# Performance work log

Hardware: AMD Instinct MI355X
Metric: run time of the kernel (lower is better)

The kernel has to match this reference:

```python
import jax, jax.numpy as jnp
import numpy as np

# CSV_Architecture_v2 layout (per frame, 130 floats):
#   hand 0 block: [0]=handedness label, [1]=handedness prob, [2:65]=21*3 coords
#   hand 1 block: [65]=handedness label, [66]=handedness prob, [67:130]=coords
POS0, PROB0 = 0, 1
POS1, PROB1 = 65, 66
HAND_LEN = 65
FRAME_LEN = 2 * HAND_LEN


def _build_swap_pattern():
    all_idxs = np.arange(FRAME_LEN)
    idxs_0 = np.arange(0, HAND_LEN)
    idxs_1 = np.arange(HAND_LEN, FRAME_LEN)
    all_idxs[idxs_0], all_idxs[idxs_1] = all_idxs[idxs_1].copy(), all_idxs[idxs_0].copy()
    return jnp.asarray(all_idxs, dtype=jnp.int32)


def setup_inputs() -> dict:
    key = jax.random.key(0)
    B, S = 256, 1024
    X = jax.random.normal(key, (B, S, FRAME_LEN), dtype=jnp.float32)
    return {"X": X, "swap_pattern": _build_swap_pattern()}


def reference(X, swap_pattern):
    # Per-frame handedness labels / probabilities.
    h0 = X[..., POS0]
    h1 = X[..., POS1]
    p0 = X[..., PROB0]
    p1 = X[..., PROB1]

    nan0 = jnp.isnan(h0)
    nan1 = jnp.isnan(h1)
    no_nan = jnp.logical_and(~nan0, ~nan1)

    one = jnp.float32(1.0)
    zero = jnp.float32(0.0)

    # skip1: hands already ordered (right label > left label)
    skip1 = h1 > h0
    # skip2: both predictions NaN -> no hands detected
    skip2 = jnp.logical_and(nan0, nan1)
    # skip3: only hand 1 present, labeled right (==1)
    skip3 = jnp.logical_and(nan0, h1 == one)
    # skip4: only hand 0 present, labeled left (==0)
    skip4 = jnp.logical_and(nan1, h0 == zero)
    eq = h0 == h1
    # skip5: both labeled left, position-0 hand has higher prob
    skip5 = no_nan & eq & (h0 == zero) & (p0 > p1)
    # skip6: both labeled right, position-1 hand has higher prob
    skip6 = no_nan & eq & (h0 == one) & (p0 < p1)

    skip = skip1 | skip2 | skip3 | skip4 | skip5 | skip6

    # Vectorized replacement of nested tf.map_fn: gather-permute the frame
    # representation where a swap is required.
    swapped = X[..., swap_pattern]  # [B, S, FRAME_LEN]
    return jnp.where(skip[..., None], X, swapped)
```

## Files before the change

kernel.cpp:

```cpp
#include <hip/hip_runtime.h>

constexpr int FRAME_LEN = 130;
constexpr int HALF      = 65;
constexpr int BLOCK     = 256;
constexpr int FPB       = 32;
constexpr int CHUNK_F   = FPB * FRAME_LEN;
constexpr int CHUNK_V4  = CHUNK_F / 4;

__device__ __forceinline__ int div130(int idx) {
    return (int)(((unsigned)idx * 8067u) >> 20);
}

__global__ __launch_bounds__(BLOCK, 8)
void hand_sorter_kernel(const float* __restrict__ X, float* __restrict__ out,
                        int n_frames) {
    __shared__ float s_buf[CHUNK_F];
    __shared__ unsigned char s_skip[FPB];

    const int t = threadIdx.x;
    const long long frame0 = (long long)blockIdx.x * FPB;
    const long long rem = (long long)n_frames - frame0;
    const int frames_here = rem < (long long)FPB ? (int)rem : FPB;
    const int nf = frames_here * FRAME_LEN;
    const int n4 = (nf + 3) >> 2;
    const long long base = frame0 * (long long)FRAME_LEN;
    const float4* __restrict__ Xv = (const float4*)(X + base);
    float4* __restrict__ Ov = (float4*)(out + base);

    for (int i = t; i < n4; i += BLOCK) {
        *(float4*)(s_buf + 4 * i) = Xv[i];
    }
    __syncthreads();

    if (t < frames_here) {
        const float* fr = s_buf + t * FRAME_LEN;
        const float h0 = fr[0];
        const float p0 = fr[1];
        const float h1 = fr[HALF];
        const float p1 = fr[HALF + 1];
        const bool nan0 = (h0 != h0);
        const bool nan1 = (h1 != h1);
        const bool no_nan = !nan0 && !nan1;
        const bool eq = (h0 == h1);
        const bool skip =
            (h1 > h0) ||
            (nan0 && nan1) ||
            (nan0 && (h1 == 1.0f)) ||
            (nan1 && (h0 == 0.0f)) ||
            (no_nan && eq && (h0 == 0.0f) && (p0 > p1)) ||
            (no_nan && eq && (h0 == 1.0f) && (p0 < p1));
        s_skip[t] = (unsigned char)skip;
    }
    __syncthreads();

    for (int i = t; i < n4; i += BLOCK) {
        const int idx = 4 * i;
        float4 v;
        float* vp = (float*)&v;
        if (idx + 3 < nf) {
#pragma unroll
            for (int e = 0; e < 4; ++e) {
                const int ide = idx + e;
                const int fl = div130(ide);
                const int jj = ide - fl * FRAME_LEN;
                int sj = jj + (s_skip[fl] ? 0 : HALF);
                if (sj >= FRAME_LEN) sj -= FRAME_LEN;
                vp[e] = s_buf[fl * FRAME_LEN + sj];
            }
            Ov[i] = v;
        } else {
            for (int e = 0; e < 4; ++e) {
                const int ide = idx + e;
                if (ide < nf) {
                    const int fl = div130(ide);
                    const int jj = ide - fl * FRAME_LEN;
                    int sj = jj + (s_skip[fl] ? 0 : HALF);
                    if (sj >= FRAME_LEN) sj -= FRAME_LEN;
                    out[base + ide] = s_buf[fl * FRAME_LEN + sj];
                }
            }
        }
    }
}

extern "C" void kernel_launch(void* const* d_in, const int* in_sizes, int n_in,
                              void* d_out, int out_size, void* d_ws, size_t ws_size,
                              hipStream_t stream) {
    const float* X = (const float*)d_in[0];
    float* out = (float*)d_out;
    const int n_frames = in_sizes[0] / FRAME_LEN;
    const int n_blocks = (n_frames + FPB - 1) / FPB;
    hand_sorter_kernel<<<n_blocks, BLOCK, 0, stream>>>(X, out, n_frames);
}
```

Measured before the change: 240.1 us.

## Drop shared-memory staging and gather directly from global memory

```diff
diff --git a/kernel.cpp b/kernel.cpp
--- a/kernel.cpp
+++ b/kernel.cpp
@@ -5,7 +5,8 @@
 constexpr int BLOCK     = 256;
 constexpr int FPB       = 32;
 constexpr int CHUNK_F   = FPB * FRAME_LEN;
-constexpr int CHUNK_V4  = CHUNK_F / 4;
+
+typedef float f4u __attribute__((ext_vector_type(4), aligned(4)));
 
 __device__ __forceinline__ int div130(int idx) {
     return (int)(((unsigned)idx * 8067u) >> 20);
@@ -14,8 +15,7 @@
 __global__ __launch_bounds__(BLOCK, 8)
 void hand_sorter_kernel(const float* __restrict__ X, float* __restrict__ out,
                         int n_frames) {
-    __shared__ float s_buf[CHUNK_F];
-    __shared__ unsigned char s_skip[FPB];
+    __shared__ int s_off[FPB];
 
     const int t = threadIdx.x;
     const long long frame0 = (long long)blockIdx.x * FPB;
@@ -24,16 +24,11 @@
     const int nf = frames_here * FRAME_LEN;
     const int n4 = (nf + 3) >> 2;
     const long long base = frame0 * (long long)FRAME_LEN;
-    const float4* __restrict__ Xv = (const float4*)(X + base);
-    float4* __restrict__ Ov = (float4*)(out + base);
-
-    for (int i = t; i < n4; i += BLOCK) {
-        *(float4*)(s_buf + 4 * i) = Xv[i];
-    }
-    __syncthreads();
+    const float* __restrict__ Xb = X + base;
+    float* __restrict__ Ob = out + base;
 
     if (t < frames_here) {
-        const float* fr = s_buf + t * FRAME_LEN;
+        const float* fr = Xb + t * FRAME_LEN;
         const float h0 = fr[0];
         const float p0 = fr[1];
         const float h1 = fr[HALF];
@@ -49,34 +44,34 @@
             (nan1 && (h0 == 0.0f)) ||
             (no_nan && eq && (h0 == 0.0f) && (p0 > p1)) ||
             (no_nan && eq && (h0 == 1.0f) && (p0 < p1));
-        s_skip[t] = (unsigned char)skip;
+        s_off[t] = skip ? 0 : HALF;
     }
     __syncthreads();
 
     for (int i = t; i < n4; i += BLOCK) {
         const int idx = 4 * i;
-        float4 v;
-        float* vp = (float*)&v;
-        if (idx + 3 < nf) {
+        const int fl = div130(idx);
+        const int jj = idx - fl * FRAME_LEN;
+        const bool same_frame = (idx + 3 < nf) && (jj <= FRAME_LEN - 4);
+        const bool no_half_cross = (jj < HALF - 3) || (jj >= HALF);
+        if (same_frame && no_half_cross) {
+            int sj = jj + s_off[fl];
+            if (sj >= FRAME_LEN) sj -= FRAME_LEN;
+            const float* src = Xb + (fl * FRAME_LEN + sj);
+            f4u v = *(const f4u*)src;
+            float4 o;
+            o.x = v.x; o.y = v.y; o.z = v.z; o.w = v.w;
+            *(float4*)(Ob + idx) = o;
+        } else {
 #pragma unroll
             for (int e = 0; e < 4; ++e) {
                 const int ide = idx + e;
-                const int fl = div130(ide);
-                const int jj = ide - fl * FRAME_LEN;
-                int sj = jj + (s_skip[fl] ? 0 : HALF);
-                if (sj >= FRAME_LEN) sj -= FRAME_LEN;
-                vp[e] = s_buf[fl * FRAME_LEN + sj];
-            }
-            Ov[i] = v;
-        } else {
-            for (int e = 0; e < 4; ++e) {
-                const int ide = idx + e;
                 if (ide < nf) {
-                    const int fl = div130(ide);
-                    const int jj = ide - fl * FRAME_LEN;
-                    int sj = jj + (s_skip[fl] ? 0 : HALF);
+                    const int fle = div130(ide);
+                    const int je = ide - fle * FRAME_LEN;
+                    int sj = je + s_off[fle];
                     if (sj >= FRAME_LEN) sj -= FRAME_LEN;
-                    out[base + ide] = s_buf[fl * FRAME_LEN + sj];
+                    Ob[ide] = Xb[fle * FRAME_LEN + sj];
                 }
             }
         }
```

Measured after the change: 268.9 us. 1.12x slower.

## Load tiles with direct global-to-LDS DMA and compute skip mask via per-wave ballot

Applied to the files above, without the earlier changes.

```diff
diff --git a/kernel.cpp b/kernel.cpp
--- a/kernel.cpp
+++ b/kernel.cpp
@@ -1,4 +1,5 @@
 #include <hip/hip_runtime.h>
+#include <stdint.h>
 
 constexpr int FRAME_LEN = 130;
 constexpr int HALF      = 65;
@@ -7,78 +8,107 @@
 constexpr int CHUNK_F   = FPB * FRAME_LEN;
 constexpr int CHUNK_V4  = CHUNK_F / 4;
 
+#define GLOBAL_AS __attribute__((address_space(1)))
+#define LDS_AS    __attribute__((address_space(3)))
+
 __device__ __forceinline__ int div130(int idx) {
     return (int)(((unsigned)idx * 8067u) >> 20);
+}
+
+__device__ __forceinline__ bool skip_pred(float h0, float p0, float h1, float p1) {
+    const bool nan0 = (h0 != h0);
+    const bool nan1 = (h1 != h1);
+    const bool no_nan = !nan0 && !nan1;
+    const bool eq = (h0 == h1);
+    return (h1 > h0) ||
+           (nan0 && nan1) ||
+           (nan0 && (h1 == 1.0f)) ||
+           (nan1 && (h0 == 0.0f)) ||
+           (no_nan && eq && (h0 == 0.0f) && (p0 > p1)) ||
+           (no_nan && eq && (h0 == 1.0f) && (p0 < p1));
 }
 
 __global__ __launch_bounds__(BLOCK, 8)
 void hand_sorter_kernel(const float* __restrict__ X, float* __restrict__ out,
                         int n_frames) {
     __shared__ float s_buf[CHUNK_F];
-    __shared__ unsigned char s_skip[FPB];
 
     const int t = threadIdx.x;
     const long long frame0 = (long long)blockIdx.x * FPB;
     const long long rem = (long long)n_frames - frame0;
     const int frames_here = rem < (long long)FPB ? (int)rem : FPB;
-    const int nf = frames_here * FRAME_LEN;
-    const int n4 = (nf + 3) >> 2;
     const long long base = frame0 * (long long)FRAME_LEN;
-    const float4* __restrict__ Xv = (const float4*)(X + base);
-    float4* __restrict__ Ov = (float4*)(out + base);
+    const float* __restrict__ Xb = X + base;
+    float* __restrict__ Ob = out + base;
 
-    for (int i = t; i < n4; i += BLOCK) {
-        *(float4*)(s_buf + 4 * i) = Xv[i];
-    }
-    __syncthreads();
+    if (frames_here == FPB) {
+        const int wbase = t & ~63;
+#pragma unroll
+        for (int k = 0; k < 4; ++k) {
+            const float* src = Xb + 4 * (k * 256 + t);
+            float* dst = s_buf + 4 * (k * 256 + wbase);
+            __builtin_amdgcn_global_load_lds(
+                (const GLOBAL_AS uint32_t*)src, (LDS_AS uint32_t*)dst, 16, 0, 0);
+        }
+        if (t < CHUNK_V4 - 1024) {
+            const float* src = Xb + 4 * (1024 + t);
+            float* dst = s_buf + 4 * 1024;
+            __builtin_amdgcn_global_load_lds(
+                (const GLOBAL_AS uint32_t*)src, (LDS_AS uint32_t*)dst, 16, 0, 0);
+        }
+        __syncthreads();
 
-    if (t < frames_here) {
-        const float* fr = s_buf + t * FRAME_LEN;
-        const float h0 = fr[0];
-        const float p0 = fr[1];
-        const float h1 = fr[HALF];
-        const float p1 = fr[HALF + 1];
-        const bool nan0 = (h0 != h0);
-        const bool nan1 = (h1 != h1);
-        const bool no_nan = !nan0 && !nan1;
-        const bool eq = (h0 == h1);
-        const bool skip =
-            (h1 > h0) ||
-            (nan0 && nan1) ||
-            (nan0 && (h1 == 1.0f)) ||
-            (nan1 && (h0 == 0.0f)) ||
-            (no_nan && eq && (h0 == 0.0f) && (p0 > p1)) ||
-            (no_nan && eq && (h0 == 1.0f) && (p0 < p1));
-        s_skip[t] = (unsigned char)skip;
-    }
-    __syncthreads();
+        const int lane = t & 63;
+        bool pred = false;
+        if (lane < FPB) {
+            const float* fr = s_buf + lane * FRAME_LEN;
+            pred = skip_pred(fr[0], fr[1], fr[HALF], fr[HALF + 1]);
+        }
+        const unsigned mask = (unsigned)__ballot(pred);
 
-    for (int i = t; i < n4; i += BLOCK) {
-        const int idx = 4 * i;
-        float4 v;
-        float* vp = (float*)&v;
-        if (idx + 3 < nf) {
+        float4* __restrict__ Ov = (float4*)Ob;
+#pragma unroll
+        for (int k = 0; k < 4; ++k) {
+            const int i = t + k * 256;
+            const int idx = 4 * i;
+            float4 v;
+            float* vp = (float*)&v;
 #pragma unroll
             for (int e = 0; e < 4; ++e) {
                 const int ide = idx + e;
                 const int fl = div130(ide);
                 const int jj = ide - fl * FRAME_LEN;
-                int sj = jj + (s_skip[fl] ? 0 : HALF);
+                int sj = jj + (((mask >> fl) & 1u) ? 0 : HALF);
                 if (sj >= FRAME_LEN) sj -= FRAME_LEN;
                 vp[e] = s_buf[fl * FRAME_LEN + sj];
             }
             Ov[i] = v;
-        } else {
+        }
+        if (t < CHUNK_V4 - 1024) {
+            const int i = t + 1024;
+            const int idx = 4 * i;
+            float4 v;
+            float* vp = (float*)&v;
+#pragma unroll
             for (int e = 0; e < 4; ++e) {
                 const int ide = idx + e;
-                if (ide < nf) {
-                    const int fl = div130(ide);
-                    const int jj = ide - fl * FRAME_LEN;
-                    int sj = jj + (s_skip[fl] ? 0 : HALF);
-                    if (sj >= FRAME_LEN) sj -= FRAME_LEN;
-                    out[base + ide] = s_buf[fl * FRAME_LEN + sj];
-                }
+                const int fl = div130(ide);
+                const int jj = ide - fl * FRAME_LEN;
+                int sj = jj + (((mask >> fl) & 1u) ? 0 : HALF);
+                if (sj >= FRAME_LEN) sj -= FRAME_LEN;
+                vp[e] = s_buf[fl * FRAME_LEN + sj];
             }
+            Ov[i] = v;
+        }
+    } else {
+        const int nf = frames_here * FRAME_LEN;
+        for (int i = t; i < nf; i += BLOCK) {
+            const int fle = div130(i);
+            const int je  = i - fle * FRAME_LEN;
+            const float* fr = Xb + fle * FRAME_LEN;
+            const bool sk = skip_pred(fr[0], fr[1], fr[HALF], fr[HALF + 1]);
+            int sj = je + (sk ? 0 : (je < HALF ? HALF : -HALF));
+            Ob[i] = fr[sj];
         }
     }
 }
```

Result: no change. 236.3 us (-1.6%).
